# Optimization experiments

Measured on AMD Instinct MI355X. Metric: run time of the kernel, lower is better.

## Reference

```python
import jax, jax.numpy as jnp
import numpy as np

NH, NKV, HD = 32, 8, 128   # query heads, kv heads, head_dim
EPS = 1e-6
ROPE_BASE = 10000.0


def setup_inputs() -> dict:
    key = jax.random.key(0)
    ks = jax.random.split(key, 5)
    B, S, H = 2, 1024, 4096
    scale = 0.02
    return {
        "x": jax.random.normal(ks[0], (B, S, H), jnp.float32),
        "wq": jax.random.normal(ks[1], (H, NH * HD), jnp.float32) * scale,
        "wk": jax.random.normal(ks[2], (H, NKV * HD), jnp.float32) * scale,
        "wv": jax.random.normal(ks[3], (H, NKV * HD), jnp.float32) * scale,
        "wo": jax.random.normal(ks[4], (NH * HD, H), jnp.float32) * scale,
        "q_norm_w": jnp.ones((HD,), jnp.float32),
        "k_norm_w": jnp.ones((HD,), jnp.float32),
    }


def _rmsnorm(t, w):
    # per-head RMSNorm over last dim (head_dim)
    var = jnp.mean(t * t, axis=-1, keepdims=True)
    return t * jax.lax.rsqrt(var + EPS) * w


def _rope(t, cos, sin):
    # t: [B,S,h,d]; cos/sin: [S, d/2] (neox / rotate-half style)
    d2 = t.shape[-1] // 2
    t1, t2 = t[..., :d2], t[..., d2:]
    c = cos[None, :, None, :]
    s = sin[None, :, None, :]
    return jnp.concatenate([t1 * c - t2 * s, t1 * s + t2 * c], axis=-1)


def reference(x, wq, wk, wv, wo, q_norm_w, k_norm_w):
    B, S, H = x.shape
    softmax_scale = HD ** (-0.5)

    q = (x @ wq).reshape(B, S, NH, HD)
    k = (x @ wk).reshape(B, S, NKV, HD)
    v = (x @ wv).reshape(B, S, NKV, HD)

    # QK RMSNorm (qwen3 use_qk_norm)
    q = _rmsnorm(q, q_norm_w)
    k = _rmsnorm(k, k_norm_w)

    # rotary embedding, base 10000
    inv_freq = 1.0 / (ROPE_BASE ** (jnp.arange(0, HD, 2, dtype=jnp.float32) / HD))
    ang = jnp.arange(S, dtype=jnp.float32)[:, None] * inv_freq[None, :]  # [S, d/2]
    cos, sin = jnp.cos(ang), jnp.sin(ang)
    q = _rope(q, cos, sin)
    k = _rope(k, cos, sin)

    # GQA: expand kv heads to match query heads
    g = NH // NKV
    k = jnp.repeat(k, g, axis=2)  # [B,S,NH,HD]
    v = jnp.repeat(v, g, axis=2)

    scores = jnp.einsum("bqhd,bkhd->bhqk", q, k) * softmax_scale
    causal = jnp.tril(jnp.ones((S, S), dtype=bool))
    scores = jnp.where(causal[None, None], scores, jnp.finfo(scores.dtype).min)
    probs = jax.nn.softmax(scores, axis=-1)
    ctx = jnp.einsum("bhqk,bkhd->bqhd", probs, v).reshape(B, S, NH * HD)
    return ctx @ wo
```

## Files before the change

kernel.cpp:

```cpp
#include <hip/hip_runtime.h>


#define NH_ 32
#define NKV_ 8
#define HD_ 128
#define SEQ_ 1024
#define HID_ 4096
#define NQKV_ 6144

typedef unsigned short u16;
typedef __bf16 bf16x8 __attribute__((ext_vector_type(8)));
typedef float f32x4 __attribute__((ext_vector_type(4)));

__device__ __forceinline__ u16 f2bf(float f) {
  unsigned int u = __float_as_uint(f);
  return (u16)((u + 0x7FFFu + ((u >> 16) & 1u)) >> 16);
}
__device__ __forceinline__ float bf2f(u16 u) {
  return __uint_as_float(((unsigned int)u) << 16);
}
__device__ __forceinline__ f32x4 mfma16(bf16x8 a, bf16x8 b, f32x4 c) {
  return __builtin_amdgcn_mfma_f32_16x16x32_bf16(a, b, c, 0, 0, 0);
}
__device__ __forceinline__ void gld16(u16* lds, const u16* g) {
  __builtin_amdgcn_global_load_lds(
      (const __attribute__((address_space(1))) unsigned int*)g,
      (__attribute__((address_space(3))) unsigned int*)lds, 16, 0, 0);
}

__global__ __launch_bounds__(256) void prep_all(
    const float* __restrict__ x, const float* __restrict__ wq,
    const float* __restrict__ wk, const float* __restrict__ wv,
    u16* __restrict__ xb, u16* __restrict__ wqkvt) {
  const int blk = blockIdx.x;
  if (blk < 4096) {
    int i = (blk * 256 + threadIdx.x) * 8;
    float4 a = *(const float4*)(x + i);
    float4 b = *(const float4*)(x + i + 4);
    u16 o[8];
    o[0] = f2bf(a.x); o[1] = f2bf(a.y); o[2] = f2bf(a.z); o[3] = f2bf(a.w);
    o[4] = f2bf(b.x); o[5] = f2bf(b.y); o[6] = f2bf(b.z); o[7] = f2bf(b.w);
    *(uint4*)(xb + i) = *(uint4*)&o[0];
    return;
  }
  __shared__ float t[32][33];
  const int tt = blk - 4096;
  const int k0 = (tt & 127) * 32;
  const int y = tt >> 7;
  const float* src;
  int ldn, n0;
  size_t dofs;
  if (y < 128) { src = wq; ldn = 4096; n0 = y * 32; dofs = 0; }
  else if (y < 160) { src = wk; ldn = 1024; n0 = (y - 128) * 32; dofs = (size_t)4096 * 4096; }
  else { src = wv; ldn = 1024; n0 = (y - 160) * 32; dofs = (size_t)5120 * 4096; }
  const int c = threadIdx.x & 31, r4 = threadIdx.x >> 5;
#pragma unroll
  for (int i = 0; i < 4; ++i) {
    int r = r4 + i * 8;
    t[r][c] = src[(size_t)(k0 + r) * ldn + n0 + c];
  }
  __syncthreads();
#pragma unroll
  for (int i = 0; i < 4; ++i) {
    int r = r4 + i * 8;
    wqkvt[dofs + (size_t)(n0 + r) * HID_ + k0 + c] = f2bf(t[c][r]);
  }
}

__global__ __launch_bounds__(256) void mid_all(
    const float* __restrict__ wo, const u16* __restrict__ QKV,
    const float* __restrict__ QW, const float* __restrict__ KW,
    u16* __restrict__ wot, u16* __restrict__ QB, u16* __restrict__ KB,
    u16* __restrict__ VT) {
  const int blk = blockIdx.x;
  if (blk < 16384) {
    __shared__ float t[32][33];
    const int k0 = (blk & 127) * 32, n0 = (blk >> 7) * 32;
    const int c = threadIdx.x & 31, r4 = threadIdx.x >> 5;
#pragma unroll
    for (int i = 0; i < 4; ++i) {
      int r = r4 + i * 8;
      t[r][c] = wo[(size_t)(k0 + r) * HID_ + n0 + c];
    }
    __syncthreads();
#pragma unroll
    for (int i = 0; i < 4; ++i) {
      int r = r4 + i * 8;
      wot[(size_t)(n0 + r) * HID_ + k0 + c] = f2bf(t[c][r]);
    }
    return;
  }
  if (blk < 36864) {
    const float QSCALE = 0.08838834764831845f * 1.4426950408889634f;
    int vec = (blk - 16384) * 4 + (threadIdx.x >> 6);
    int lane = threadIdx.x & 63;
    const u16* src;
    u16* dst;
    const float* nw;
    int m;
    float outsc;
    if (vec < 65536) {
      m = vec >> 5;
      int hh = vec & 31;
      src = QKV + (size_t)m * NQKV_ + hh * 128;
      int b = m >> 10, s = m & 1023;
      dst = QB + (size_t)((b * NH_ + hh) * SEQ_ + s) * HD_;
      nw = QW;
      outsc = QSCALE;
    } else {
      int vk = vec - 65536;
      m = vk >> 3;
      int kvh = vk & 7;
      src = QKV + (size_t)m * NQKV_ + 4096 + kvh * 128;
      int b = m >> 10, s = m & 1023;
      dst = KB + (size_t)((b * NKV_ + kvh) * SEQ_ + s) * HD_;
      nw = KW;
      outsc = 1.0f;
    }
    float t1 = bf2f(src[lane]), t2 = bf2f(src[lane + 64]);
    float ss = t1 * t1 + t2 * t2;
#pragma unroll
    for (int off = 32; off >= 1; off >>= 1) ss += __shfl_xor(ss, off);
    float scale = rsqrtf(ss * (1.0f / 128.0f) + 1e-6f) * outsc;
    float n1 = t1 * scale * nw[lane];
    float n2 = t2 * scale * nw[lane + 64];
    int spos = m & 1023;
    float invf = powf(10000.0f, -(float)lane * (1.0f / 64.0f));
    float ang = (float)spos * invf;
    float sn, cs;
    sincosf(ang, &sn, &cs);
    dst[lane] = f2bf(n1 * cs - n2 * sn);
    dst[lane + 64] = f2bf(n1 * sn + n2 * cs);
    return;
  }
  {
    __shared__ u16 t[32][33];
    const int tt = blk - 36864;
    const int s0 = (tt & 31) * 32, d0 = ((tt >> 5) & 3) * 32;
    const int bkvh = tt >> 7;
    const int b = bkvh >> 3, kvh = bkvh & 7;
    const int c = threadIdx.x & 31, r8 = threadIdx.x >> 5;
#pragma unroll
    for (int i = 0; i < 4; ++i) {
      int r = r8 + i * 8;
      t[r][c] =
          QKV[(size_t)(b * SEQ_ + s0 + r) * NQKV_ + 5120 + kvh * 128 + d0 + c];
    }
    __syncthreads();
#pragma unroll
    for (int i = 0; i < 4; ++i) {
      int r = r8 + i * 8;
      VT[(size_t)(bkvh * HD_ + d0 + r) * SEQ_ + s0 + c] = t[c][r];
    }
  }
}

template <bool F32OUT>
__global__ __launch_bounds__(256) void gemm_bt(const u16* __restrict__ A,
                                               const u16* __restrict__ Bt,
                                               void* __restrict__ Cv, int K,
                                               int ldc) {
  __shared__ u16 As[128 * 32];
  __shared__ u16 Bs[128 * 32];
  const int bn = blockIdx.x, bm = blockIdx.y;
  const int tid = threadIdx.x, lane = tid & 63, w = tid >> 6;
  const int wr = w >> 1, wc = w & 1, ln = lane & 15, quad = lane >> 4;

  const int srow = w * 32 + (lane >> 2);
  const int skk = (lane & 3) * 8;
  const u16* ag = A + (size_t)(bm * 128 + srow) * K + skk;
  const u16* bg = Bt + (size_t)(bn * 128 + srow) * K + skk;
  u16* asd = &As[w * 1024];
  u16* bsd = &Bs[w * 1024];

  f32x4 acc[4][4];
#pragma unroll
  for (int i = 0; i < 4; ++i)
#pragma unroll
    for (int j = 0; j < 4; ++j)
#pragma unroll
      for (int r = 0; r < 4; ++r) acc[i][j][r] = 0.0f;

  for (int kb = 0; kb < K / 32; ++kb) {
    gld16(asd, ag);
    gld16(asd + 512, ag + 16 * (size_t)K);
    gld16(bsd, bg);
    gld16(bsd + 512, bg + 16 * (size_t)K);
    ag += 32;
    bg += 32;
    __syncthreads();
    bf16x8 af[4], bfr[4];
#pragma unroll
    for (int i = 0; i < 4; ++i)
      af[i] = *(const bf16x8*)&As[(wr * 64 + i * 16 + ln) * 32 + quad * 8];
#pragma unroll
    for (int j = 0; j < 4; ++j)
      bfr[j] = *(const bf16x8*)&Bs[(wc * 64 + j * 16 + ln) * 32 + quad * 8];
#pragma unroll
    for (int i = 0; i < 4; ++i)
#pragma unroll
      for (int j = 0; j < 4; ++j) acc[i][j] = mfma16(af[i], bfr[j], acc[i][j]);
    __syncthreads();
  }
#pragma unroll
  for (int i = 0; i < 4; ++i) {
#pragma unroll
    for (int r = 0; r < 4; ++r) {
      int grow = bm * 128 + wr * 64 + i * 16 + quad * 4 + r;
      int gcol = bn * 128 + wc * 64 + ln;
      if (F32OUT) {
        float* dst = (float*)Cv + (size_t)grow * ldc + gcol;
#pragma unroll
        for (int j = 0; j < 4; ++j) dst[j * 16] = acc[i][j][r];
      } else {
        u16* dst = (u16*)Cv + (size_t)grow * ldc + gcol;
#pragma unroll
        for (int j = 0; j < 4; ++j) dst[j * 16] = f2bf(acc[i][j][r]);
      }
    }
  }
}

__global__ __launch_bounds__(256) void flash_attn(
    const u16* __restrict__ QB, const u16* __restrict__ KB,
    const u16* __restrict__ VT, u16* __restrict__ CTX) {
  __shared__ u16 Ks[4][64][32];
  __shared__ u16 Vs[2][128][32];
  __shared__ u16 Pl[4][16][72];

  const int bid = blockIdx.x;
  const int qt = 15 - (bid >> 6);
  const int h = bid & 31, b = (bid >> 5) & 1;
  const int kvh = h >> 2;
  const int tid = threadIdx.x, w = tid >> 6, lane = tid & 63;
  const int ln = lane & 15, quad = lane >> 4;
  const int l4 = lane >> 2, l4r = lane & 3;

  const u16* qbase =
      QB + (size_t)((b * NH_ + h) * SEQ_ + qt * 64 + w * 16 + ln) * HD_;
  bf16x8 qf[4];
#pragma unroll
  for (int kc = 0; kc < 4; ++kc)
    qf[kc] = *(const bf16x8*)(qbase + kc * 32 + quad * 8);

  f32x4 o[8];
#pragma unroll
  for (int t = 0; t < 8; ++t)
#pragma unroll
    for (int r = 0; r < 4; ++r) o[t][r] = 0.0f;
  float m_r[4] = {-3e38f, -3e38f, -3e38f, -3e38f};
  float l_r[4] = {0.0f, 0.0f, 0.0f, 0.0f};

  const u16* krow =
      KB + (size_t)((b * NKV_ + kvh) * SEQ_ + w * 16 + l4) * HD_ + l4r * 8;
  const u16* vrow =
      VT + (size_t)((b * NKV_ + kvh) * HD_ + w * 32 + l4) * SEQ_ + l4r * 8;
  const int pswz = ((ln >> 3) & 1) << 3;

  for (int kt = 0; kt <= qt; ++kt) {
    const int key0 = kt * 64;
#pragma unroll
    for (int i = 0; i < 4; ++i)
      gld16(&Ks[i][w * 16][0], krow + (size_t)key0 * HD_ + i * 32);
#pragma unroll
    for (int i = 0; i < 4; ++i)
      gld16(&Vs[i & 1][w * 32 + (i >> 1) * 16][0],
            vrow + (size_t)(i >> 1) * 16 * SEQ_ + key0 + (i & 1) * 32);
    __syncthreads();

    f32x4 sc[4];
#pragma unroll
    for (int t2 = 0; t2 < 4; ++t2) {
#pragma unroll
      for (int r = 0; r < 4; ++r) sc[t2][r] = 0.0f;
#pragma unroll
      for (int kc = 0; kc < 4; ++kc) {
        bf16x8 kf = *(const bf16x8*)&Ks[kc][t2 * 16 + ln][quad * 8];
        sc[t2] = mfma16(qf[kc], kf, sc[t2]);
      }
    }

    const bool diag = (kt == qt);
    float p[4][4], alpha[4];
#pragma unroll
    for (int r = 0; r < 4; ++r) {
      float s0 = sc[0][r], s1 = sc[1][r], s2 = sc[2][r], s3 = sc[3][r];
      if (diag) {
        const int qi = qt * 64 + w * 16 + quad * 4 + r;
        if (key0 + ln > qi) s0 = -3e38f;
        if (key0 + 16 + ln > qi) s1 = -3e38f;
        if (key0 + 32 + ln > qi) s2 = -3e38f;
        if (key0 + 48 + ln > qi) s3 = -3e38f;
      }
      float mx = fmaxf(fmaxf(s0, s1), fmaxf(s2, s3));
#pragma unroll
      for (int off = 1; off < 16; off <<= 1) mx = fmaxf(mx, __shfl_xor(mx, off));
      float mnew = fmaxf(m_r[r], mx);
      alpha[r] = exp2f(m_r[r] - mnew);
      p[0][r] = exp2f(s0 - mnew);
      p[1][r] = exp2f(s1 - mnew);
      p[2][r] = exp2f(s2 - mnew);
      p[3][r] = exp2f(s3 - mnew);
      float rs = p[0][r] + p[1][r] + p[2][r] + p[3][r];
#pragma unroll
      for (int off = 1; off < 16; off <<= 1) rs += __shfl_xor(rs, off);
      l_r[r] = l_r[r] * alpha[r] + rs;
      m_r[r] = mnew;
    }
#pragma unroll
    for (int t = 0; t < 8; ++t)
#pragma unroll
      for (int r = 0; r < 4; ++r) o[t][r] *= alpha[r];

#pragma unroll
    for (int r = 0; r < 4; ++r) {
      const int row = quad * 4 + r;
      const int wswz = ((row >> 3) & 1) << 3;
#pragma unroll
      for (int t2 = 0; t2 < 4; ++t2)
        Pl[w][row][(t2 * 16 + ln) ^ wswz] = f2bf(p[t2][r]);
    }
    bf16x8 af0 = *(const bf16x8*)&Pl[w][ln][(quad * 8) ^ pswz];
    bf16x8 af1 = *(const bf16x8*)&Pl[w][ln][32 + ((quad * 8) ^ pswz)];
#pragma unroll
    for (int t = 0; t < 8; ++t) {
      bf16x8 vf0 = *(const bf16x8*)&Vs[0][t * 16 + ln][quad * 8];
      o[t] = mfma16(af0, vf0, o[t]);
      bf16x8 vf1 = *(const bf16x8*)&Vs[1][t * 16 + ln][quad * 8];
      o[t] = mfma16(af1, vf1, o[t]);
    }
    __syncthreads();
  }

#pragma unroll
  for (int r = 0; r < 4; ++r) {
    float inv_l = 1.0f / l_r[r];
    int srow = qt * 64 + w * 16 + quad * 4 + r;
    u16* dst = CTX + (size_t)(b * SEQ_ + srow) * (NH_ * HD_) + h * HD_;
#pragma unroll
    for (int t = 0; t < 8; ++t) dst[t * 16 + ln] = f2bf(o[t][r] * inv_l);
  }
}

extern "C" void kernel_launch(void* const* d_in, const int* in_sizes, int n_in,
                              void* d_out, int out_size, void* d_ws,
                              size_t ws_size, hipStream_t stream) {
  const float* x = (const float*)d_in[0];
  const float* wq = (const float*)d_in[1];
  const float* wk = (const float*)d_in[2];
  const float* wv = (const float*)d_in[3];
  const float* wo = (const float*)d_in[4];
  const float* qw = (const float*)d_in[5];
  const float* kw = (const float*)d_in[6];
  float* out = (float*)d_out;
  char* ws = (char*)d_ws;
  const size_t MB = 1024 * 1024;

  u16* wqkvt = (u16*)ws;
  u16* wot = (u16*)ws;
  u16* xb = (u16*)(ws + 48 * MB);
  u16* qkv = (u16*)(ws + 64 * MB);
  u16* ctx = (u16*)(ws + 64 * MB);
  u16* qb = (u16*)(ws + 88 * MB);
  u16* kb = (u16*)(ws + 104 * MB);
  u16* vt = (u16*)(ws + 108 * MB);

  prep_all<<<dim3(28672), 256, 0, stream>>>(x, wq, wk, wv, xb, wqkvt);
  gemm_bt<false><<<dim3(48, 16), 256, 0, stream>>>(xb, wqkvt, qkv, 4096, 6144);
  mid_all<<<dim3(38912), 256, 0, stream>>>(wo, qkv, qw, kw, wot, qb, kb, vt);
  flash_attn<<<dim3(1024), 256, 0, stream>>>(qb, kb, vt, ctx);
  gemm_bt<true><<<dim3(32, 16), 256, 0, stream>>>(ctx, wot, out, 4096, 4096);
}
```

Measured before the change: 528.9 us.

## Replace 128x128 GEMM with pipelined 256x256 tile kernel using swizzled LDS

Replaces the simple 128x128 single-buffered bf16 GEMM with a 256x256-tile, 512-thread kernel. It uses a 64-wide K step, double-buffered LDS with XOR-swizzled columns to avoid bank conflicts, and async global-to-LDS loads interleaved with MFMA phases. It also adds s_setprio around the MFMA blocks and a block-index remap for L2 locality. The aim is more data reuse per tile and overlap of memory traffic with compute in both projection GEMMs. In exchange, the larger tile gives far fewer blocks (192 and 128), which may underfill the 256 CUs and raises register pressure.

```diff
diff --git a/kernel.cpp b/kernel.cpp
--- a/kernel.cpp
+++ b/kernel.cpp
@@ -155,71 +155,238 @@
   }
 }
 
+
+#define RD_A(QMOFS, ACOL)                                                  \
+  _Pragma("unroll") for (int mfl = 0; mfl < 4; ++mfl) af[mfl] =            \
+      *(const bf16x8*)&aS[(arow0 + (QMOFS) + mfl * 16) * 64 + (ACOL)];
+#define RD_B(ACOL)                                                         \
+  _Pragma("unroll") for (int nf = 0; nf < 4; ++nf) bf[nf] =                \
+      *(const bf16x8*)&bS[(brow0 + nf * 16) * 64 + (ACOL)];
+#define MM(QB)                                                             \
+  _Pragma("unroll") for (int mfl = 0; mfl < 4; ++mfl)                      \
+  _Pragma("unroll") for (int nf = 0; nf < 4; ++nf) acc[(QB) + mfl][nf] =   \
+      mfma16(af[mfl], bf[nf], acc[(QB) + mfl][nf]);
+#define BAR() __builtin_amdgcn_s_barrier()
+#define PRIO1() __builtin_amdgcn_s_setprio(1)
+#define PRIO0() __builtin_amdgcn_s_setprio(0)
+#define SCB() __builtin_amdgcn_sched_barrier(0)
+
 template <bool F32OUT>
-__global__ __launch_bounds__(256) void gemm_bt(const u16* __restrict__ A,
-                                               const u16* __restrict__ Bt,
-                                               void* __restrict__ Cv, int K,
-                                               int ldc) {
-  __shared__ u16 As[128 * 32];
-  __shared__ u16 Bs[128 * 32];
-  const int bn = blockIdx.x, bm = blockIdx.y;
-  const int tid = threadIdx.x, lane = tid & 63, w = tid >> 6;
-  const int wr = w >> 1, wc = w & 1, ln = lane & 15, quad = lane >> 4;
-
-  const int srow = w * 32 + (lane >> 2);
-  const int skk = (lane & 3) * 8;
-  const u16* ag = A + (size_t)(bm * 128 + srow) * K + skk;
-  const u16* bg = Bt + (size_t)(bn * 128 + srow) * K + skk;
-  u16* asd = &As[w * 1024];
-  u16* bsd = &Bs[w * 1024];
-
-  f32x4 acc[4][4];
-#pragma unroll
-  for (int i = 0; i < 4; ++i)
+__global__ __launch_bounds__(512, 2) void gemm256(
+    const u16* __restrict__ A, const u16* __restrict__ Bt,
+    void* __restrict__ Cv, int K, int ldc, int nbn) {
+  __shared__ __align__(16) u16 As[2][16384];
+  __shared__ __align__(16) u16 Bs[2][16384];
+
+  const int cpx = gridDim.x >> 3;
+  const int sw = (blockIdx.x & 7) * cpx + (blockIdx.x >> 3);
+  const int bm = sw / nbn, bn = sw % nbn;
+
+  const int tid = threadIdx.x;
+  const int w = tid >> 6, lane = tid & 63;
+  const int wm = w >> 2, wn = w & 3;
+  const int ln = lane & 15, quad = lane >> 4;
+
+  const int srow = lane >> 3;
+  const int scol = ((lane & 7) ^ srow) * 8;
+  const u16 *ag0, *ag1, *ag2, *ag3, *bg0, *bg1, *bg2, *bg3;
+  {
+    const size_t ra = (size_t)(bm * 256 + w * 8 + srow) * K + scol;
+    ag0 = A + ra;
+    ag1 = A + ra + (size_t)64 * K;
+    ag2 = A + ra + (size_t)128 * K;
+    ag3 = A + ra + (size_t)192 * K;
+    const size_t rb = (size_t)(bn * 256 + w * 8 + srow) * K + scol;
+    bg0 = Bt + rb;
+    bg1 = Bt + rb + (size_t)64 * K;
+    bg2 = Bt + rb + (size_t)128 * K;
+    bg3 = Bt + rb + (size_t)192 * K;
+  }
+  u16* const aw = &As[0][0] + w * 512;
+  u16* const bw = &Bs[0][0] + w * 512;
+
+  const int acol0 = (quad * 8) ^ ((ln & 7) << 3);
+  const int acol1 = (32 + quad * 8) ^ ((ln & 7) << 3);
+  const int arow0 = wm * 128 + ln;
+  const int brow0 = wn * 64 + ln;
+
+  f32x4 acc[8][4];
+#pragma unroll
+  for (int i = 0; i < 8; ++i)
 #pragma unroll
     for (int j = 0; j < 4; ++j)
 #pragma unroll
       for (int r = 0; r < 4; ++r) acc[i][j][r] = 0.0f;
 
-  for (int kb = 0; kb < K / 32; ++kb) {
-    gld16(asd, ag);
-    gld16(asd + 512, ag + 16 * (size_t)K);
-    gld16(bsd, bg);
-    gld16(bsd + 512, bg + 16 * (size_t)K);
-    ag += 32;
-    bg += 32;
-    __syncthreads();
-    bf16x8 af[4], bfr[4];
-#pragma unroll
-    for (int i = 0; i < 4; ++i)
-      af[i] = *(const bf16x8*)&As[(wr * 64 + i * 16 + ln) * 32 + quad * 8];
-#pragma unroll
-    for (int j = 0; j < 4; ++j)
-      bfr[j] = *(const bf16x8*)&Bs[(wc * 64 + j * 16 + ln) * 32 + quad * 8];
-#pragma unroll
-    for (int i = 0; i < 4; ++i)
-#pragma unroll
-      for (int j = 0; j < 4; ++j) acc[i][j] = mfma16(af[i], bfr[j], acc[i][j]);
-    __syncthreads();
-  }
-#pragma unroll
-  for (int i = 0; i < 4; ++i) {
+  const int nt = K >> 6;
+
+  gld16(aw + 0, ag0);
+  gld16(aw + 8192, ag2);
+  gld16(bw + 0, bg0);
+  gld16(bw + 4096, bg1);
+  gld16(bw + 8192, bg2);
+  gld16(bw + 12288, bg3);
+  gld16(aw + 4096, ag1);
+  gld16(aw + 12288, ag3);
+  gld16(aw + 16384 + 0, ag0 + 64);
+  gld16(aw + 16384 + 8192, ag2 + 64);
+  ag0 += 128; ag2 += 128; ag1 += 64; ag3 += 64;
+  bg0 += 64; bg1 += 64; bg2 += 64; bg3 += 64;
+  asm volatile("s_waitcnt vmcnt(4)" ::: "memory");
+  BAR();
+  SCB();
+
+  int sofs = 0;
+#pragma unroll 1
+  for (int t = 0; t < nt - 2; ++t) {
+    const int so = sofs, sn = sofs ^ 16384;
+    const u16* aS = &As[0][0] + so;
+    const u16* bS = &Bs[0][0] + so;
+    bf16x8 af[4], bf[4];
+    RD_B(acol0);
+    RD_A(0, acol0);
+    gld16(bw + sn + 0, bg0);
+    gld16(bw + sn + 4096, bg1);
+    BAR();
+    PRIO1();
+    MM(0);
+    PRIO0();
+    asm volatile("s_waitcnt vmcnt(4)" ::: "memory");
+    BAR();
+    SCB();
+    RD_A(64, acol0);
+    gld16(bw + sn + 8192, bg2);
+    gld16(bw + sn + 12288, bg3);
+    BAR();
+    PRIO1();
+    MM(4);
+    PRIO0();
+    BAR();
+    RD_B(acol1);
+    RD_A(0, acol1);
+    gld16(aw + sn + 4096, ag1);
+    gld16(aw + sn + 12288, ag3);
+    BAR();
+    PRIO1();
+    MM(0);
+    PRIO0();
+    BAR();
+    RD_A(64, acol1);
+    gld16(aw + so + 0, ag0);
+    gld16(aw + so + 8192, ag2);
+    BAR();
+    PRIO1();
+    MM(4);
+    PRIO0();
+    asm volatile("s_waitcnt vmcnt(4)" ::: "memory");
+    BAR();
+    SCB();
+    ag0 += 64; ag1 += 64; ag2 += 64; ag3 += 64;
+    bg0 += 64; bg1 += 64; bg2 += 64; bg3 += 64;
+    sofs ^= 16384;
+  }
+  {
+    const int so = sofs, sn = sofs ^ 16384;
+    const u16* aS = &As[0][0] + so;
+    const u16* bS = &Bs[0][0] + so;
+    bf16x8 af[4], bf[4];
+    RD_B(acol0);
+    RD_A(0, acol0);
+    gld16(bw + sn + 0, bg0);
+    gld16(bw + sn + 4096, bg1);
+    BAR();
+    PRIO1();
+    MM(0);
+    PRIO0();
+    asm volatile("s_waitcnt vmcnt(4)" ::: "memory");
+    BAR();
+    SCB();
+    RD_A(64, acol0);
+    gld16(bw + sn + 8192, bg2);
+    gld16(bw + sn + 12288, bg3);
+    BAR();
+    PRIO1();
+    MM(4);
+    PRIO0();
+    BAR();
+    RD_B(acol1);
+    RD_A(0, acol1);
+    gld16(aw + sn + 4096, ag1);
+    gld16(aw + sn + 12288, ag3);
+    BAR();
+    PRIO1();
+    MM(0);
+    PRIO0();
+    BAR();
+    RD_A(64, acol1);
+    BAR();
+    PRIO1();
+    MM(4);
+    PRIO0();
+    asm volatile("s_waitcnt vmcnt(2)" ::: "memory");
+    BAR();
+    SCB();
+    sofs ^= 16384;
+  }
+  {
+    const int so = sofs;
+    const u16* aS = &As[0][0] + so;
+    const u16* bS = &Bs[0][0] + so;
+    bf16x8 af[4], bf[4];
+    RD_B(acol0);
+    RD_A(0, acol0);
+    BAR();
+    PRIO1();
+    MM(0);
+    PRIO0();
+    asm volatile("s_waitcnt vmcnt(0)" ::: "memory");
+    BAR();
+    SCB();
+    RD_A(64, acol0);
+    BAR();
+    PRIO1();
+    MM(4);
+    PRIO0();
+    BAR();
+    RD_B(acol1);
+    RD_A(0, acol1);
+    BAR();
+    PRIO1();
+    MM(0);
+    PRIO0();
+    BAR();
+    RD_A(64, acol1);
+    PRIO1();
+    MM(4);
+    PRIO0();
+  }
+
+  const int gcol = bn * 256 + wn * 64 + ln;
+#pragma unroll
+  for (int mfg = 0; mfg < 8; ++mfg) {
 #pragma unroll
     for (int r = 0; r < 4; ++r) {
-      int grow = bm * 128 + wr * 64 + i * 16 + quad * 4 + r;
-      int gcol = bn * 128 + wc * 64 + ln;
+      const int grow = bm * 256 + wm * 128 + mfg * 16 + quad * 4 + r;
       if (F32OUT) {
         float* dst = (float*)Cv + (size_t)grow * ldc + gcol;
 #pragma unroll
-        for (int j = 0; j < 4; ++j) dst[j * 16] = acc[i][j][r];
+        for (int nf = 0; nf < 4; ++nf) dst[nf * 16] = acc[mfg][nf][r];
       } else {
         u16* dst = (u16*)Cv + (size_t)grow * ldc + gcol;
 #pragma unroll
-        for (int j = 0; j < 4; ++j) dst[j * 16] = f2bf(acc[i][j][r]);
+        for (int nf = 0; nf < 4; ++nf) dst[nf * 16] = f2bf(acc[mfg][nf][r]);
       }
     }
   }
 }
+
+#undef RD_A
+#undef RD_B
+#undef MM
+#undef BAR
+#undef PRIO1
+#undef PRIO0
+#undef SCB
 
 __global__ __launch_bounds__(256) void flash_attn(
     const u16* __restrict__ QB, const u16* __restrict__ KB,
@@ -366,8 +533,8 @@
   u16* vt = (u16*)(ws + 108 * MB);
 
   prep_all<<<dim3(28672), 256, 0, stream>>>(x, wq, wk, wv, xb, wqkvt);
-  gemm_bt<false><<<dim3(48, 16), 256, 0, stream>>>(xb, wqkvt, qkv, 4096, 6144);
+  gemm256<false><<<dim3(192), 512, 0, stream>>>(xb, wqkvt, qkv, 4096, 6144, 24);
   mid_all<<<dim3(38912), 256, 0, stream>>>(wo, qkv, qw, kw, wot, qb, kb, vt);
   flash_attn<<<dim3(1024), 256, 0, stream>>>(qb, kb, vt, ctx);
-  gemm_bt<true><<<dim3(32, 16), 256, 0, stream>>>(ctx, wot, out, 4096, 4096);
-}
+  gemm256<true><<<dim3(128), 512, 0, stream>>>(ctx, wot, out, 4096, 4096, 16);
+}
```

New measurement: 554.5 us. +4.8%, slower.

## Replace GEMM with 8-wave double-buffered pipelined kernel with swizzled LDS

Applied to the files above, without the earlier changes.

Replaces the simple 128x128 bf16 GEMM with a 512-thread kernel that uses 128xBN tiles (BN=384 for the QKV projection, 256 for the output projection) and a K-step of 64. Global-to-LDS loads are double buffered and split into phases that are interleaved with MFMA work, using explicit waitcnt and barriers and raised wave priority during the MFMAs. LDS is XOR-swizzled to avoid bank conflicts, and block indices are remapped for L2 locality. Tile sizes, grid shapes and waitcnt counts are hardcoded, so the kernel relies on these problem shapes, and the hand-written wait counts risk subtle races if any count is wrong.

```diff
diff --git a/kernel.cpp b/kernel.cpp
--- a/kernel.cpp
+++ b/kernel.cpp
@@ -155,71 +155,209 @@
   }
 }
 
-template <bool F32OUT>
-__global__ __launch_bounds__(256) void gemm_bt(const u16* __restrict__ A,
-                                               const u16* __restrict__ Bt,
-                                               void* __restrict__ Cv, int K,
-                                               int ldc) {
-  __shared__ u16 As[128 * 32];
-  __shared__ u16 Bs[128 * 32];
-  const int bn = blockIdx.x, bm = blockIdx.y;
-  const int tid = threadIdx.x, lane = tid & 63, w = tid >> 6;
-  const int wr = w >> 1, wc = w & 1, ln = lane & 15, quad = lane >> 4;
-
-  const int srow = w * 32 + (lane >> 2);
-  const int skk = (lane & 3) * 8;
-  const u16* ag = A + (size_t)(bm * 128 + srow) * K + skk;
-  const u16* bg = Bt + (size_t)(bn * 128 + srow) * K + skk;
-  u16* asd = &As[w * 1024];
-  u16* bsd = &Bs[w * 1024];
-
-  f32x4 acc[4][4];
-#pragma unroll
-  for (int i = 0; i < 4; ++i)
-#pragma unroll
-    for (int j = 0; j < 4; ++j)
-#pragma unroll
-      for (int r = 0; r < 4; ++r) acc[i][j][r] = 0.0f;
-
-  for (int kb = 0; kb < K / 32; ++kb) {
-    gld16(asd, ag);
-    gld16(asd + 512, ag + 16 * (size_t)K);
-    gld16(bsd, bg);
-    gld16(bsd + 512, bg + 16 * (size_t)K);
-    ag += 32;
-    bg += 32;
-    __syncthreads();
-    bf16x8 af[4], bfr[4];
-#pragma unroll
-    for (int i = 0; i < 4; ++i)
-      af[i] = *(const bf16x8*)&As[(wr * 64 + i * 16 + ln) * 32 + quad * 8];
-#pragma unroll
-    for (int j = 0; j < 4; ++j)
-      bfr[j] = *(const bf16x8*)&Bs[(wc * 64 + j * 16 + ln) * 32 + quad * 8];
-#pragma unroll
-    for (int i = 0; i < 4; ++i)
-#pragma unroll
-      for (int j = 0; j < 4; ++j) acc[i][j] = mfma16(af[i], bfr[j], acc[i][j]);
-    __syncthreads();
-  }
-#pragma unroll
-  for (int i = 0; i < 4; ++i) {
+
+#define BAR() __builtin_amdgcn_s_barrier()
+#define PRIO1() __builtin_amdgcn_s_setprio(1)
+#define PRIO0() __builtin_amdgcn_s_setprio(0)
+#define LGKM0() asm volatile("s_waitcnt lgkmcnt(0)" ::: "memory")
+#define LGKM8() asm volatile("s_waitcnt lgkmcnt(8)" ::: "memory")
+#define VM(n) asm volatile("s_waitcnt vmcnt(" #n ")" ::: "memory")
+
+#define STGA(slot, l, koff) \
+  gld16(&L[(slot)*SLOT + (l)*4096 + wofs], aB + (size_t)(l)*64*K + (koff))
+#define STGB(slot, l, koff) \
+  gld16(&L[(slot)*SLOT + 8192 + (l)*4096 + wofs], bB + (size_t)(l)*64*K + (koff))
+
+#define PH_READS(p)                                                       \
+  if ((p) == 0) {                                                         \
+    _Pragma("unroll") for (int m = 0; m < 4; ++m)                         \
+        af[0][m] = *(const bf16x8*)&Ls[aro + m * 1024 + acS0];            \
+    _Pragma("unroll") for (int m = 0; m < 4; ++m)                         \
+        af[1][m] = *(const bf16x8*)&Ls[aro + m * 1024 + acS1];            \
+  }                                                                       \
+  bf[0][0] = *(const bf16x8*)&Ls[bro + (p)*8192 + acS0];                  \
+  bf[0][1] = *(const bf16x8*)&Ls[bro + (p)*8192 + 4096 + acS0];           \
+  bf[1][0] = *(const bf16x8*)&Ls[bro + (p)*8192 + acS1];                  \
+  bf[1][1] = *(const bf16x8*)&Ls[bro + (p)*8192 + 4096 + acS1];
+
+#define PH_MM(p)                                                          \
+  _Pragma("unroll") for (int kk = 0; kk < 2; ++kk)                        \
+  _Pragma("unroll") for (int m = 0; m < 4; ++m)                           \
+  _Pragma("unroll") for (int j = 0; j < 2; ++j)                           \
+      acc[m][2 * (p) + j] = mfma16(af[kk][m], bf[kk][j], acc[m][2 * (p) + j]);
+
+template <int NF, bool F32OUT>
+__global__ __launch_bounds__(512, 2) void gemm8p(
+    const u16* __restrict__ A, const u16* __restrict__ Bt,
+    void* __restrict__ Cv, const int K, const int ldc) {
+  constexpr int BN = NF * 64;
+  constexpr int NP = NF / 2;
+  constexpr int SLOT = (128 + BN) * 64;
+  __shared__ __align__(16) u16 L[2 * SLOT];
+
+  const int sw = (blockIdx.x & 7) * 32 + (blockIdx.x >> 3);
+  const int bm = sw >> 4, bn = sw & 15;
+
+  const int tid = threadIdx.x, w = tid >> 6, lane = tid & 63;
+  const int wm = w >> 2, wn = w & 3;
+  const int ln = lane & 15, quad = lane >> 4;
+
+  const int srow = lane >> 3;
+  const int scol = ((lane & 7) ^ srow) * 8;
+  const u16* aB = A + (size_t)(bm * 128 + w * 8 + srow) * K + scol;
+  const u16* bB = Bt + (size_t)(bn * BN + w * 8 + srow) * K + scol;
+  const int wofs = w * 512;
+
+  const int acS0 = (quad * 8) ^ ((ln & 7) << 3);
+  const int acS1 = (32 + quad * 8) ^ ((ln & 7) << 3);
+  const int aro = (wm * 64 + ln) * 64;
+  const int bro = 8192 + (wn * 16 + ln) * 64;
+
+  f32x4 acc[4][NF];
+#pragma unroll
+  for (int m = 0; m < 4; ++m)
+#pragma unroll
+    for (int f = 0; f < NF; ++f)
+#pragma unroll
+      for (int r = 0; r < 4; ++r) acc[m][f][r] = 0.0f;
+
+  const int nt = K >> 6;
+
+  STGA(0, 0, 0);
+  STGA(0, 1, 0);
+#pragma unroll
+  for (int l = 0; l < NF; ++l) STGB(0, l, 0);
+  STGA(1, 0, 64);
+  STGA(1, 1, 64);
+  STGB(1, 0, 64);
+  if constexpr (NP == 3) {
+    STGB(1, 1, 64); STGB(1, 2, 64); STGB(1, 3, 64);
+    VM(6);
+  } else {
+    STGB(1, 1, 64);
+    VM(4);
+  }
+  BAR();
+
+  bf16x8 af[2][4], bf[2][2];
+  int s = 0;
+#pragma unroll 2
+  for (int t = 0; t < nt - 2; ++t) {
+    const u16* Ls = &L[s * SLOT];
+    const int sn = s ^ 1;
+    const int k1 = (t + 1) << 6, k2 = (t + 2) << 6;
+    PH_READS(0);
+    STGB(sn, NF - 2, k1);
+    STGB(sn, NF - 1, k1);
+    LGKM8();
+    BAR();
+    LGKM0();
+    PRIO1(); PH_MM(0); PRIO0();
+    if constexpr (NP == 2) VM(6);
+    BAR();
+    PH_READS(1);
+    STGA(s, 0, k2);
+    STGA(s, 1, k2);
+    STGB(s, 0, k2);
+    if constexpr (NP == 2) STGB(s, 1, k2);
+    BAR();
+    LGKM0();
+    PRIO1(); PH_MM(1); PRIO0();
+    if constexpr (NP == 3) { VM(11); } else { VM(6); }
+    BAR();
+    if constexpr (NP == 3) {
+      PH_READS(2);
+      STGB(s, 1, k2);
+      STGB(s, 2, k2);
+      STGB(s, 3, k2);
+      BAR();
+      LGKM0();
+      PRIO1(); PH_MM(2); PRIO0();
+      VM(8);
+      BAR();
+    }
+    s = sn;
+  }
+  {
+    const u16* Ls = &L[s * SLOT];
+    const int sn = s ^ 1;
+    const int k1 = (nt - 1) << 6;
+    PH_READS(0);
+    STGB(sn, NF - 2, k1);
+    STGB(sn, NF - 1, k1);
+    LGKM8();
+    BAR();
+    LGKM0();
+    PRIO1(); PH_MM(0); PRIO0();
+    if constexpr (NP == 2) VM(6);
+    BAR();
+    PH_READS(1);
+    BAR();
+    LGKM0();
+    PRIO1(); PH_MM(1); PRIO0();
+    if constexpr (NP == 3) { VM(8); } else { VM(2); }
+    BAR();
+    if constexpr (NP == 3) {
+      PH_READS(2);
+      BAR();
+      LGKM0();
+      PRIO1(); PH_MM(2); PRIO0();
+      VM(2);
+      BAR();
+    }
+    s = sn;
+  }
+  {
+    const u16* Ls = &L[s * SLOT];
+    PH_READS(0);
+    BAR();
+    LGKM0();
+    PRIO1(); PH_MM(0); PRIO0();
+    if constexpr (NP == 2) VM(0);
+    BAR();
+    PH_READS(1);
+    BAR();
+    LGKM0();
+    PRIO1(); PH_MM(1); PRIO0();
+    if constexpr (NP == 3) {
+      VM(0);
+      BAR();
+      PH_READS(2);
+      BAR();
+      LGKM0();
+      PRIO1(); PH_MM(2); PRIO0();
+    }
+  }
+
+  const int colb = bn * BN + wn * 16 + ln;
+#pragma unroll
+  for (int m = 0; m < 4; ++m) {
 #pragma unroll
     for (int r = 0; r < 4; ++r) {
-      int grow = bm * 128 + wr * 64 + i * 16 + quad * 4 + r;
-      int gcol = bn * 128 + wc * 64 + ln;
+      const int grow = bm * 128 + wm * 64 + m * 16 + quad * 4 + r;
       if (F32OUT) {
-        float* dst = (float*)Cv + (size_t)grow * ldc + gcol;
-#pragma unroll
-        for (int j = 0; j < 4; ++j) dst[j * 16] = acc[i][j][r];
+        float* dst = (float*)Cv + (size_t)grow * ldc + colb;
+#pragma unroll
+        for (int f = 0; f < NF; ++f) dst[f * 64] = acc[m][f][r];
       } else {
-        u16* dst = (u16*)Cv + (size_t)grow * ldc + gcol;
-#pragma unroll
-        for (int j = 0; j < 4; ++j) dst[j * 16] = f2bf(acc[i][j][r]);
+        u16* dst = (u16*)Cv + (size_t)grow * ldc + colb;
+#pragma unroll
+        for (int f = 0; f < NF; ++f) dst[f * 64] = f2bf(acc[m][f][r]);
       }
     }
   }
 }
+
+#undef PH_READS
+#undef PH_MM
+#undef STGA
+#undef STGB
+#undef BAR
+#undef PRIO1
+#undef PRIO0
+#undef LGKM0
+#undef LGKM8
+#undef VM
 
 __global__ __launch_bounds__(256) void flash_attn(
     const u16* __restrict__ QB, const u16* __restrict__ KB,
@@ -366,8 +504,8 @@
   u16* vt = (u16*)(ws + 108 * MB);
 
   prep_all<<<dim3(28672), 256, 0, stream>>>(x, wq, wk, wv, xb, wqkvt);
-  gemm_bt<false><<<dim3(48, 16), 256, 0, stream>>>(xb, wqkvt, qkv, 4096, 6144);
+  gemm8p<6, false><<<dim3(256), 512, 0, stream>>>(xb, wqkvt, qkv, 4096, 6144);
   mid_all<<<dim3(38912), 256, 0, stream>>>(wo, qkv, qw, kw, wot, qb, kb, vt);
   flash_attn<<<dim3(1024), 256, 0, stream>>>(qb, kb, vt, ctx);
-  gemm_bt<true><<<dim3(32, 16), 256, 0, stream>>>(ctx, wot, out, 4096, 4096);
-}
+  gemm8p<4, true><<<dim3(256), 512, 0, stream>>>(ctx, wot, out, 4096, 4096);
+}
```

New measurement: 462.4 us. 12.6% less time.

## Replace GEMM kernel with double-buffered 8-wave pipelined MFMA GEMM

Applied to the files above, without the earlier changes.

Both projection GEMMs move from a simple 128x128 tile, K=32, single-buffer kernel to a 512-thread kernel with larger tiles (128x384 or 128x256) and K=64 steps. The new kernel uses double-buffered LDS with an XOR-swizzled layout, keeps loads in flight with explicit vmcnt waits, raises wave priority around MFMA bursts, and remaps block IDs so tiles are visited in a grouped order. The goal is to hide global-load latency, cut LDS bank conflicts and barrier stalls, and improve L2 reuse. The cost is more registers and LDS per block and fragile hand-tuned wait counts that depend on K being a multiple of 128.

```diff
diff --git a/kernel.cpp b/kernel.cpp
--- a/kernel.cpp
+++ b/kernel.cpp
@@ -155,71 +155,198 @@
   }
 }
 
-template <bool F32OUT>
-__global__ __launch_bounds__(256) void gemm_bt(const u16* __restrict__ A,
-                                               const u16* __restrict__ Bt,
-                                               void* __restrict__ Cv, int K,
-                                               int ldc) {
-  __shared__ u16 As[128 * 32];
-  __shared__ u16 Bs[128 * 32];
-  const int bn = blockIdx.x, bm = blockIdx.y;
-  const int tid = threadIdx.x, lane = tid & 63, w = tid >> 6;
-  const int wr = w >> 1, wc = w & 1, ln = lane & 15, quad = lane >> 4;
-
-  const int srow = w * 32 + (lane >> 2);
-  const int skk = (lane & 3) * 8;
-  const u16* ag = A + (size_t)(bm * 128 + srow) * K + skk;
-  const u16* bg = Bt + (size_t)(bn * 128 + srow) * K + skk;
-  u16* asd = &As[w * 1024];
-  u16* bsd = &Bs[w * 1024];
-
-  f32x4 acc[4][4];
-#pragma unroll
-  for (int i = 0; i < 4; ++i)
-#pragma unroll
-    for (int j = 0; j < 4; ++j)
-#pragma unroll
-      for (int r = 0; r < 4; ++r) acc[i][j][r] = 0.0f;
-
-  for (int kb = 0; kb < K / 32; ++kb) {
-    gld16(asd, ag);
-    gld16(asd + 512, ag + 16 * (size_t)K);
-    gld16(bsd, bg);
-    gld16(bsd + 512, bg + 16 * (size_t)K);
-    ag += 32;
-    bg += 32;
-    __syncthreads();
-    bf16x8 af[4], bfr[4];
-#pragma unroll
-    for (int i = 0; i < 4; ++i)
-      af[i] = *(const bf16x8*)&As[(wr * 64 + i * 16 + ln) * 32 + quad * 8];
-#pragma unroll
-    for (int j = 0; j < 4; ++j)
-      bfr[j] = *(const bf16x8*)&Bs[(wc * 64 + j * 16 + ln) * 32 + quad * 8];
-#pragma unroll
-    for (int i = 0; i < 4; ++i)
-#pragma unroll
-      for (int j = 0; j < 4; ++j) acc[i][j] = mfma16(af[i], bfr[j], acc[i][j]);
-    __syncthreads();
-  }
-#pragma unroll
-  for (int i = 0; i < 4; ++i) {
+
+#define BAR() __builtin_amdgcn_s_barrier()
+#define PRIO1() __builtin_amdgcn_s_setprio(1)
+#define PRIO0() __builtin_amdgcn_s_setprio(0)
+#define VM(n) asm volatile("s_waitcnt vmcnt(" #n ")" ::: "memory")
+
+#define STGA(slot, l, koff) \
+  gld16(&L[(slot)*SLOT + (l)*4096 + wofs], aB + (size_t)(l)*64*K + (koff))
+#define STGB(slot, l, koff) \
+  gld16(&L[(slot)*SLOT + 8192 + (l)*4096 + wofs], bB + (size_t)(l)*64*K + (koff))
+
+#define RDB(dst, Ls, p)                                                   \
+  dst[0][0] = *(const bf16x8*)&(Ls)[bro + (2*(p))*4096 + acS0];           \
+  dst[0][1] = *(const bf16x8*)&(Ls)[bro + (2*(p)+1)*4096 + acS0];         \
+  dst[1][0] = *(const bf16x8*)&(Ls)[bro + (2*(p))*4096 + acS1];           \
+  dst[1][1] = *(const bf16x8*)&(Ls)[bro + (2*(p)+1)*4096 + acS1];
+
+#define RDA(dst, Ls)                                                      \
+  _Pragma("unroll") for (int m_ = 0; m_ < 4; ++m_) {                      \
+    dst[0][m_] = *(const bf16x8*)&(Ls)[aro + m_*1024 + acS0];             \
+    dst[1][m_] = *(const bf16x8*)&(Ls)[aro + m_*1024 + acS1];             \
+  }
+
+#define MMp(p, bq, AF)                                                    \
+  _Pragma("unroll") for (int kk = 0; kk < 2; ++kk)                        \
+  _Pragma("unroll") for (int m = 0; m < 4; ++m)                           \
+  _Pragma("unroll") for (int j = 0; j < 2; ++j)                           \
+    acc[m][2*(p)+j] = mfma16(AF[kk][m], bq[kk][j], acc[m][2*(p)+j]);
+
+#define TILE3(SO, SN, AFc, AFn, K1, K2)                                   \
+  {                                                                       \
+    const u16* Ls = &L[(SO)*SLOT];                                        \
+    bf16x8 bq0[2][2], bq1[2][2], bq2[2][2];                               \
+    RDB(bq0, Ls, 0); RDB(bq1, Ls, 1);                                     \
+    STGB((SN), 4, (K1)); STGB((SN), 5, (K1));                             \
+    BAR(); PRIO1(); MMp(0, bq0, AFc); PRIO0(); BAR();                     \
+    RDB(bq2, Ls, 2);                                                      \
+    STGA((SO), 0, (K2)); STGA((SO), 1, (K2)); STGB((SO), 0, (K2));        \
+    BAR(); PRIO1(); MMp(1, bq1, AFc); PRIO0(); VM(8); BAR();              \
+    RDA(AFn, (&L[(SN)*SLOT]));                                            \
+    STGB((SO), 1, (K2)); STGB((SO), 2, (K2)); STGB((SO), 3, (K2));        \
+    BAR(); PRIO1(); MMp(2, bq2, AFc); PRIO0(); VM(6); BAR();              \
+  }
+
+#define TILE2(SO, SN, AFc, AFn, K1, K2)                                   \
+  {                                                                       \
+    const u16* Ls = &L[(SO)*SLOT];                                        \
+    bf16x8 bq0[2][2], bq1[2][2];                                          \
+    RDB(bq0, Ls, 0); RDB(bq1, Ls, 1);                                     \
+    STGB((SN), 2, (K1)); STGB((SN), 3, (K1));                             \
+    BAR(); PRIO1(); MMp(0, bq0, AFc); PRIO0(); VM(2); BAR();              \
+    RDA(AFn, (&L[(SN)*SLOT]));                                            \
+    STGA((SO), 0, (K2)); STGA((SO), 1, (K2));                             \
+    STGB((SO), 0, (K2)); STGB((SO), 1, (K2));                             \
+    BAR(); PRIO1(); MMp(1, bq1, AFc); PRIO0(); VM(4); BAR();              \
+  }
+
+template <int NF, bool F32OUT>
+__global__ __launch_bounds__(512, 2) void gemm8p(
+    const u16* __restrict__ A_, const u16* __restrict__ Bt,
+    void* __restrict__ Cv, const int K, const int ldc) {
+  constexpr int NP = NF / 2;
+  constexpr int SLOT = (128 + NF * 64) * 64;
+  __shared__ __align__(16) u16 L[2 * SLOT];
+
+  const int sw = (blockIdx.x & 7) * 32 + (blockIdx.x >> 3);
+  const int bm = sw >> 4, bn = sw & 15;
+
+  const int tid = threadIdx.x, w = tid >> 6, lane = tid & 63;
+  const int wm = w >> 2, wn = w & 3;
+  const int ln = lane & 15, quad = lane >> 4;
+
+  const int srow = lane >> 3;
+  const int scol = ((lane & 7) ^ srow) * 8;
+  const u16* aB = A_ + (size_t)(bm * 128 + w * 8 + srow) * K + scol;
+  const u16* bB = Bt + (size_t)(bn * (NF * 64) + w * 8 + srow) * K + scol;
+  const int wofs = w * 512;
+
+  const int acS0 = (quad * 8) ^ ((ln & 7) << 3);
+  const int acS1 = (32 + quad * 8) ^ ((ln & 7) << 3);
+  const int aro = (wm * 64 + ln) * 64;
+  const int bro = 8192 + (wn * 16 + ln) * 64;
+
+  f32x4 acc[4][NF];
+#pragma unroll
+  for (int m = 0; m < 4; ++m)
+#pragma unroll
+    for (int f = 0; f < NF; ++f)
+#pragma unroll
+      for (int r = 0; r < 4; ++r) acc[m][f][r] = 0.0f;
+
+  const int nt = K >> 6;
+  bf16x8 af0[2][4], af1[2][4];
+
+  if constexpr (NP == 3) {
+    STGA(0, 0, 0); STGA(0, 1, 0);
+    STGB(0, 0, 0); STGB(0, 1, 0); STGB(0, 2, 0);
+    STGB(0, 3, 0); STGB(0, 4, 0); STGB(0, 5, 0);
+    STGA(1, 0, 64); STGA(1, 1, 64); STGB(1, 0, 64);
+    STGB(1, 1, 64); STGB(1, 2, 64); STGB(1, 3, 64);
+    VM(6); BAR();
+    RDA(af0, (&L[0]));
+    int kof = 0;
+#pragma unroll 1
+    for (int it = 0; it < (nt - 2) / 2; ++it) {
+      TILE3(0, 1, af0, af1, kof + 64, kof + 128);
+      TILE3(1, 0, af1, af0, kof + 128, kof + 192);
+      kof += 128;
+    }
+    {
+      const u16* Ls = &L[0];
+      bf16x8 bq0[2][2], bq1[2][2], bq2[2][2];
+      RDB(bq0, Ls, 0); RDB(bq1, Ls, 1);
+      STGB(1, 4, kof + 64); STGB(1, 5, kof + 64);
+      BAR(); PRIO1(); MMp(0, bq0, af0); PRIO0(); BAR();
+      RDB(bq2, Ls, 2);
+      BAR(); PRIO1(); MMp(1, bq1, af0); PRIO0(); VM(5); BAR();
+      RDA(af1, (&L[SLOT]));
+      BAR(); PRIO1(); MMp(2, bq2, af0); PRIO0(); VM(0); BAR();
+    }
+    {
+      const u16* Ls = &L[SLOT];
+      bf16x8 bq0[2][2], bq1[2][2], bq2[2][2];
+      RDB(bq0, Ls, 0); RDB(bq1, Ls, 1); RDB(bq2, Ls, 2);
+      BAR();
+      PRIO1();
+      MMp(0, bq0, af1); MMp(1, bq1, af1); MMp(2, bq2, af1);
+      PRIO0();
+    }
+  } else {
+    STGA(0, 0, 0); STGA(0, 1, 0);
+    STGB(0, 0, 0); STGB(0, 1, 0); STGB(0, 2, 0); STGB(0, 3, 0);
+    STGA(1, 0, 64); STGA(1, 1, 64); STGB(1, 0, 64); STGB(1, 1, 64);
+    VM(4); BAR();
+    RDA(af0, (&L[0]));
+    int kof = 0;
+#pragma unroll 1
+    for (int it = 0; it < (nt - 2) / 2; ++it) {
+      TILE2(0, 1, af0, af1, kof + 64, kof + 128);
+      TILE2(1, 0, af1, af0, kof + 128, kof + 192);
+      kof += 128;
+    }
+    {
+      const u16* Ls = &L[0];
+      bf16x8 bq0[2][2], bq1[2][2];
+      RDB(bq0, Ls, 0); RDB(bq1, Ls, 1);
+      STGB(1, 2, kof + 64); STGB(1, 3, kof + 64);
+      BAR(); PRIO1(); MMp(0, bq0, af0); PRIO0(); VM(2); BAR();
+      RDA(af1, (&L[SLOT]));
+      BAR(); PRIO1(); MMp(1, bq1, af0); PRIO0(); VM(0); BAR();
+    }
+    {
+      const u16* Ls = &L[SLOT];
+      bf16x8 bq0[2][2], bq1[2][2];
+      RDB(bq0, Ls, 0); RDB(bq1, Ls, 1);
+      BAR();
+      PRIO1();
+      MMp(0, bq0, af1); MMp(1, bq1, af1);
+      PRIO0();
+    }
+  }
+
+  const int colb = bn * (NF * 64) + wn * 16 + ln;
+#pragma unroll
+  for (int m = 0; m < 4; ++m) {
 #pragma unroll
     for (int r = 0; r < 4; ++r) {
-      int grow = bm * 128 + wr * 64 + i * 16 + quad * 4 + r;
-      int gcol = bn * 128 + wc * 64 + ln;
+      const int grow = bm * 128 + wm * 64 + m * 16 + quad * 4 + r;
       if (F32OUT) {
-        float* dst = (float*)Cv + (size_t)grow * ldc + gcol;
-#pragma unroll
-        for (int j = 0; j < 4; ++j) dst[j * 16] = acc[i][j][r];
+        float* dst = (float*)Cv + (size_t)grow * ldc + colb;
+#pragma unroll
+        for (int f = 0; f < NF; ++f) dst[f * 64] = acc[m][f][r];
       } else {
-        u16* dst = (u16*)Cv + (size_t)grow * ldc + gcol;
-#pragma unroll
-        for (int j = 0; j < 4; ++j) dst[j * 16] = f2bf(acc[i][j][r]);
+        u16* dst = (u16*)Cv + (size_t)grow * ldc + colb;
+#pragma unroll
+        for (int f = 0; f < NF; ++f) dst[f * 64] = f2bf(acc[m][f][r]);
       }
     }
   }
 }
+
+#undef TILE3
+#undef TILE2
+#undef RDB
+#undef RDA
+#undef MMp
+#undef STGA
+#undef STGB
+#undef BAR
+#undef PRIO1
+#undef PRIO0
+#undef VM
 
 __global__ __launch_bounds__(256) void flash_attn(
     const u16* __restrict__ QB, const u16* __restrict__ KB,
@@ -366,8 +493,8 @@
   u16* vt = (u16*)(ws + 108 * MB);
 
   prep_all<<<dim3(28672), 256, 0, stream>>>(x, wq, wk, wv, xb, wqkvt);
-  gemm_bt<false><<<dim3(48, 16), 256, 0, stream>>>(xb, wqkvt, qkv, 4096, 6144);
+  gemm8p<6, false><<<dim3(256), 512, 0, stream>>>(xb, wqkvt, qkv, 4096, 6144);
   mid_all<<<dim3(38912), 256, 0, stream>>>(wo, qkv, qw, kw, wot, qb, kb, vt);
   flash_attn<<<dim3(1024), 256, 0, stream>>>(qb, kb, vt, ctx);
-  gemm_bt<true><<<dim3(32, 16), 256, 0, stream>>>(ctx, wot, out, 4096, 4096);
-}
+  gemm8p<4, true><<<dim3(256), 512, 0, stream>>>(ctx, wot, out, 4096, 4096);
+}
```

Measured after the change: 448.7 us. 15.2% less time.
